# Kernel tuning notes

Hardware: AMD Instinct MI355X
Metric: run time of the kernel (lower is better)

Reference implementation:

```python
import jax, jax.numpy as jnp
import numpy as np

BETA = 0.9
THRESHOLD = 1.0


def setup_inputs() -> dict:
    key = jax.random.key(0)
    k1, k2 = jax.random.split(key)
    T, N_IN, N_OUT = 1024, 4096, 4096
    x = jax.random.normal(k1, (T, N_IN), dtype=jnp.float32)
    # fc1 weight initialized uniform[0,1), shape [out, in] like nn.Linear
    W = jax.random.uniform(k2, (N_OUT, N_IN), dtype=jnp.float32)
    return {"x": x, "W": W}


def reference(x, W):
    # Precompute the batched linear projection over all timesteps: [T, N_OUT]
    cur = jnp.einsum('ti,oi->to', x, W)
    mem0 = jnp.zeros((W.shape[0],), dtype=x.dtype)

    def step(mem, c):
        # snntorch Leaky, reset_mechanism='subtract':
        # reset is computed from the PREVIOUS membrane potential (detached)
        reset = (mem > THRESHOLD).astype(mem.dtype)
        mem_new = BETA * mem + c - reset * THRESHOLD
        spk = (mem_new > THRESHOLD).astype(mem.dtype)
        return mem_new, (spk, mem_new)

    _, (spk_rec, mem_rec) = jax.lax.scan(step, mem0, cur)
    return spk_rec, mem_rec
```

## Files before the change

kernel.cpp:

```cpp
#include <hip/hip_runtime.h>
#include <hip/hip_bf16.h>
#include <stdint.h>


typedef __attribute__((ext_vector_type(8))) short bf16x8;
typedef __attribute__((ext_vector_type(4))) float floatx4;

#define T_STEPS 1024
#define N_IN    4096
#define N_OUT   4096

#define GM 64
#define GN 128
#define BKK 64

#define CHUNK 32
#define NCHUNK (T_STEPS / CHUNK)

#define PH_T 128
#define NB_N 16
#define TP   130

#define TN ((size_t)T_STEPS * N_OUT)

__device__ __forceinline__ unsigned short f2bf_rne(float f) {
    unsigned int u = __builtin_bit_cast(unsigned int, f);
    unsigned int r = 0x7FFFu + ((u >> 16) & 1u);
    return (unsigned short)((u + r) >> 16);
}

__global__ __launch_bounds__(256) void cvt_kernel(const float4* __restrict__ in,
                                                  ushort4* __restrict__ out, int n4) {
    int i = blockIdx.x * blockDim.x + threadIdx.x;
    if (i < n4) {
        float4 v = in[i];
        ushort4 o;
        o.x = f2bf_rne(v.x);
        o.y = f2bf_rne(v.y);
        o.z = f2bf_rne(v.z);
        o.w = f2bf_rne(v.w);
        out[i] = o;
    }
}

__device__ __forceinline__ void gload16(const void* g, void* l) {
    __builtin_amdgcn_global_load_lds((const __attribute__((address_space(1))) void*)g,
                                     (__attribute__((address_space(3))) void*)l,
                                     16, 0, 0);
}

__global__ __launch_bounds__(256) void gemm_bt(const short* __restrict__ A,
                                               const short* __restrict__ B,
                                               float* __restrict__ P,
                                               int kLen) {
    __shared__ short sA[GM * BKK];
    __shared__ short sB[GN * BKK];

    const int tid  = threadIdx.x;
    const int lane = tid & 63;
    const int wv   = tid >> 6;
    const int wn   = wv * 32;

    const int bid    = blockIdx.x;
    const int z      = bid >> 9;
    const int n_tile = bid & 31;
    const int m_tile = (bid >> 5) & 15;
    const long bm = (long)m_tile * GM;
    const long bn = (long)n_tile * GN;
    const int kBeg = z * kLen;
    const int kEnd = kBeg + kLen;
    float* __restrict__ Pz = P + (size_t)z * TN;

    floatx4 acc[4][2] = {};

    const int srow = tid >> 3;
    const int scol = (tid & 7) * 8;
    const short* gA[2];
    const short* gB[4];
    short* lA[2];
    short* lB[4];
#pragma unroll
    for (int p = 0; p < 2; ++p) {
        gA[p] = A + (bm + p * 32 + srow) * (long)N_IN + scol;
        lA[p] = sA + p * 2048 + tid * 8;
    }
#pragma unroll
    for (int p = 0; p < 4; ++p) {
        gB[p] = B + (bn + p * 32 + srow) * (long)N_IN + scol;
        lB[p] = sB + p * 2048 + tid * 8;
    }

    const int fm  = lane & 15;
    const int fko = (lane >> 4) * 8;

    for (int k0 = kBeg; k0 < kEnd; k0 += BKK) {
#pragma unroll
        for (int p = 0; p < 2; ++p) gload16(gA[p] + k0, lA[p]);
#pragma unroll
        for (int p = 0; p < 4; ++p) gload16(gB[p] + k0, lB[p]);
        __syncthreads();

#pragma unroll
        for (int ks = 0; ks < 2; ++ks) {
            bf16x8 af[4], bfr[2];
#pragma unroll
            for (int i = 0; i < 4; ++i)
                af[i] = *(const bf16x8*)(sA + (i * 16 + fm) * 64 + ks * 32 + fko);
#pragma unroll
            for (int j = 0; j < 2; ++j)
                bfr[j] = *(const bf16x8*)(sB + (wn + j * 16 + fm) * 64 + ks * 32 + fko);
#pragma unroll
            for (int i = 0; i < 4; ++i)
#pragma unroll
                for (int j = 0; j < 2; ++j)
                    acc[i][j] = __builtin_amdgcn_mfma_f32_16x16x32_bf16(
                        af[i], bfr[j], acc[i][j], 0, 0, 0);
        }
        __syncthreads();
    }

    const int cn = lane & 15;
    const int cm = (lane >> 4) * 4;
#pragma unroll
    for (int i = 0; i < 4; ++i)
#pragma unroll
        for (int j = 0; j < 2; ++j)
#pragma unroll
            for (int r = 0; r < 4; ++r)
                Pz[(bm + i * 16 + cm + r) * (long)N_OUT + bn + wn + j * 16 + cn] =
                    acc[i][j][r];
}

template <int NPART>
__global__ __launch_bounds__(256) void boundary_kernel(const float* __restrict__ P,
                                                       float* __restrict__ bnd) {
    __shared__ float ring[2][NB_N * TP];

    const int tid  = threadIdx.x;
    const int wv   = tid >> 6;
    const int lane = tid & 63;
    const int n0   = blockIdx.x * NB_N;

    const int pn = lane & 15;
    const int tr = lane >> 4;

    float mem = 0.0f;

    if (wv < 3) {
        float v0[11], v1[11];
        int gidx[11];
#pragma unroll
        for (int i = 0; i < 11; ++i) {
            int g = wv + 3 * i;
            gidx[i] = g;
            if (g < 32) {
                size_t idx = (size_t)(g * 4 + tr) * N_OUT + n0 + pn;
                v0[i] = P[idx];
                if (NPART == 2) v1[i] = P[TN + idx];
            }
        }
#pragma unroll
        for (int i = 0; i < 11; ++i)
            if (gidx[i] < 32)
                ring[0][pn * TP + gidx[i] * 4 + tr] =
                    (NPART == 2) ? (v0[i] + v1[i]) : v0[i];
    }
    __syncthreads();

    for (int ph = 0; ph < T_STEPS / PH_T; ++ph) {
        if (wv < 3) {
            if (ph + 1 < T_STEPS / PH_T) {
                const size_t tb = (size_t)(ph + 1) * PH_T;
                float v0[11], v1[11];
                int gidx[11];
#pragma unroll
                for (int i = 0; i < 11; ++i) {
                    int g = wv + 3 * i;
                    gidx[i] = g;
                    if (g < 32) {
                        size_t idx = (tb + g * 4 + tr) * N_OUT + n0 + pn;
                        v0[i] = P[idx];
                        if (NPART == 2) v1[i] = P[TN + idx];
                    }
                }
#pragma unroll
                for (int i = 0; i < 11; ++i)
                    if (gidx[i] < 32)
                        ring[(ph + 1) & 1][pn * TP + gidx[i] * 4 + tr] =
                            (NPART == 2) ? (v0[i] + v1[i]) : v0[i];
            }
        } else {
            const float* base = &ring[ph & 1][pn * TP];
#pragma unroll
            for (int sub = 0; sub < 4; ++sub) {
                if (lane < 16)
                    bnd[(size_t)(ph * 4 + sub) * N_OUT + n0 + pn] = mem;
                float2 buf[16];
#pragma unroll
                for (int q = 0; q < 16; ++q)
                    buf[q] = *(const float2*)&base[sub * 32 + q * 2];
#pragma unroll
                for (int q = 0; q < 16; ++q) {
                    {
                        float rst = mem > 1.0f ? 1.0f : 0.0f;
                        mem = fmaf(0.9f, mem, buf[q].x) - rst;
                    }
                    {
                        float rst = mem > 1.0f ? 1.0f : 0.0f;
                        mem = fmaf(0.9f, mem, buf[q].y) - rst;
                    }
                }
            }
        }
        __syncthreads();
    }
}

template <int NPART>
__global__ __launch_bounds__(256) void replay_kernel(const float* __restrict__ P,
                                                     const float* __restrict__ bnd,
                                                     float* __restrict__ out) {
    const int lane = threadIdx.x & 63;
    const int w    = threadIdx.x >> 6;
    const int n    = blockIdx.x * 64 + lane;
    const int c    = blockIdx.y * 4 + w;
    float* __restrict__ spk  = out;
    float* __restrict__ memo = out + TN;

    float mem = bnd[(size_t)c * N_OUT + n];
    const float* __restrict__ p0 = P + (size_t)c * CHUNK * N_OUT + n;
    const float* __restrict__ p1 = p0 + TN;

    float v[CHUNK];
#pragma unroll
    for (int j = 0; j < CHUNK; ++j) {
        float a = p0[(size_t)j * N_OUT];
        if (NPART == 2) a += p1[(size_t)j * N_OUT];
        v[j] = a;
    }

#pragma unroll
    for (int j = 0; j < CHUNK; ++j) {
        float rst = mem > 1.0f ? 1.0f : 0.0f;
        mem = fmaf(0.9f, mem, v[j]) - rst;
        size_t idx = (size_t)(c * CHUNK + j) * N_OUT + n;
        spk[idx]  = mem > 1.0f ? 1.0f : 0.0f;
        memo[idx] = mem;
    }
}

extern "C" void kernel_launch(void* const* d_in, const int* in_sizes, int n_in,
                              void* d_out, int out_size, void* d_ws, size_t ws_size,
                              hipStream_t stream) {
    const float* x = (const float*)d_in[0];
    const float* W = (const float*)d_in[1];
    float* out = (float*)d_out;

    char* ws = (char*)d_ws;
    const size_t xbBytes = (size_t)T_STEPS * N_IN * 2;
    const size_t WbBytes = (size_t)N_OUT * N_IN * 2;
    const size_t PBytes  = TN * 4;
    const size_t bndBytes = (size_t)NCHUNK * N_OUT * 4;
    short* xb = (short*)ws;
    short* Wb = (short*)(ws + xbBytes);
    float* P  = (float*)(ws + xbBytes + WbBytes);

    const int S = (ws_size >= xbBytes + WbBytes + 2 * PBytes + bndBytes) ? 2 : 1;
    float* bnd = (float*)(ws + xbBytes + WbBytes + (size_t)S * PBytes);

    {
        int n4 = T_STEPS * N_IN / 4;
        cvt_kernel<<<n4 / 256, 256, 0, stream>>>((const float4*)x, (ushort4*)xb, n4);
    }
    {
        int n4 = N_OUT * N_IN / 4;
        cvt_kernel<<<n4 / 256, 256, 0, stream>>>((const float4*)W, (ushort4*)Wb, n4);
    }

    gemm_bt<<<512 * S, 256, 0, stream>>>(xb, Wb, P, N_IN / S);

    if (S == 2) {
        boundary_kernel<2><<<N_OUT / NB_N, 256, 0, stream>>>(P, bnd);
        replay_kernel<2><<<dim3(N_OUT / 64, NCHUNK / 4), 256, 0, stream>>>(P, bnd, out);
    } else {
        boundary_kernel<1><<<N_OUT / NB_N, 256, 0, stream>>>(P, bnd);
        replay_kernel<1><<<dim3(N_OUT / 64, NCHUNK / 4), 256, 0, stream>>>(P, bnd, out);
    }
}
```

Baseline: 203.2 us.

## Fuse boundary scan and replay into one scan kernel writing outputs directly

The separate boundary and replay kernels are merged into a single scan kernel. Scan lanes store each membrane value into a shared-memory ring, and loader waves write spike and membrane outputs for the previous phase while they prefetch the next phase. This removes the second read of P, the boundary buffer and one launch. Split-K is also raised to 4 partitions when the workspace allows, which gives the GEMM more blocks but means the scan has to read and sum more partial buffers. Output writes are now issued by only 3 waves per block of 16 columns, with stores 16 floats wide, which may give poorly coalesced write bandwidth.

```diff
diff --git a/kernel.cpp b/kernel.cpp
--- a/kernel.cpp
+++ b/kernel.cpp
@@ -14,10 +14,8 @@
 #define GN 128
 #define BKK 64
 
-#define CHUNK 32
-#define NCHUNK (T_STEPS / CHUNK)
-
 #define PH_T 128
+#define NPH  (T_STEPS / PH_T)
 #define NB_N 16
 #define TP   130
 
@@ -132,9 +130,10 @@
 }
 
 template <int NPART>
-__global__ __launch_bounds__(256) void boundary_kernel(const float* __restrict__ P,
-                                                       float* __restrict__ bnd) {
-    __shared__ float ring[2][NB_N * TP];
+__global__ __launch_bounds__(256) void scan_kernel(const float* __restrict__ P,
+                                                   float* __restrict__ out) {
+    __shared__ float ringCur[2][NB_N * TP];
+    __shared__ float ringMem[2][NB_N * TP];
 
     const int tid  = threadIdx.x;
     const int wv   = tid >> 6;
@@ -147,105 +146,116 @@
     float mem = 0.0f;
 
     if (wv < 3) {
-        float v0[11], v1[11];
-        int gidx[11];
+        float v[NPART][11];
+        int gi[11];
 #pragma unroll
         for (int i = 0; i < 11; ++i) {
             int g = wv + 3 * i;
-            gidx[i] = g;
+            gi[i] = g;
             if (g < 32) {
                 size_t idx = (size_t)(g * 4 + tr) * N_OUT + n0 + pn;
-                v0[i] = P[idx];
-                if (NPART == 2) v1[i] = P[TN + idx];
+#pragma unroll
+                for (int zz = 0; zz < NPART; ++zz) v[zz][i] = P[(size_t)zz * TN + idx];
             }
         }
 #pragma unroll
         for (int i = 0; i < 11; ++i)
-            if (gidx[i] < 32)
-                ring[0][pn * TP + gidx[i] * 4 + tr] =
-                    (NPART == 2) ? (v0[i] + v1[i]) : v0[i];
+            if (gi[i] < 32) {
+                float s = v[0][i];
+#pragma unroll
+                for (int zz = 1; zz < NPART; ++zz) s += v[zz][i];
+                ringCur[0][pn * TP + gi[i] * 4 + tr] = s;
+            }
     }
     __syncthreads();
 
-    for (int ph = 0; ph < T_STEPS / PH_T; ++ph) {
+    for (int ph = 0; ph < NPH; ++ph) {
         if (wv < 3) {
-            if (ph + 1 < T_STEPS / PH_T) {
-                const size_t tb = (size_t)(ph + 1) * PH_T;
-                float v0[11], v1[11];
-                int gidx[11];
+            if (ph >= 1) {
+                const float* mr = ringMem[(ph - 1) & 1];
+                const size_t tb = (size_t)(ph - 1) * PH_T;
+                float mv[11];
+                int gi[11];
 #pragma unroll
                 for (int i = 0; i < 11; ++i) {
                     int g = wv + 3 * i;
-                    gidx[i] = g;
+                    gi[i] = g;
+                    if (g < 32) mv[i] = mr[pn * TP + g * 4 + tr];
+                }
+#pragma unroll
+                for (int i = 0; i < 11; ++i)
+                    if (gi[i] < 32) {
+                        size_t idx = (tb + gi[i] * 4 + tr) * N_OUT + n0 + pn;
+                        out[idx]      = mv[i] > 1.0f ? 1.0f : 0.0f;
+                        out[TN + idx] = mv[i];
+                    }
+            }
+            if (ph + 1 < NPH) {
+                const size_t tb = (size_t)(ph + 1) * PH_T;
+                float v[NPART][11];
+                int gi[11];
+#pragma unroll
+                for (int i = 0; i < 11; ++i) {
+                    int g = wv + 3 * i;
+                    gi[i] = g;
                     if (g < 32) {
                         size_t idx = (tb + g * 4 + tr) * N_OUT + n0 + pn;
-                        v0[i] = P[idx];
-                        if (NPART == 2) v1[i] = P[TN + idx];
+#pragma unroll
+                        for (int zz = 0; zz < NPART; ++zz)
+                            v[zz][i] = P[(size_t)zz * TN + idx];
                     }
                 }
 #pragma unroll
                 for (int i = 0; i < 11; ++i)
-                    if (gidx[i] < 32)
-                        ring[(ph + 1) & 1][pn * TP + gidx[i] * 4 + tr] =
-                            (NPART == 2) ? (v0[i] + v1[i]) : v0[i];
-            }
-        } else {
-            const float* base = &ring[ph & 1][pn * TP];
+                    if (gi[i] < 32) {
+                        float s = v[0][i];
+#pragma unroll
+                        for (int zz = 1; zz < NPART; ++zz) s += v[zz][i];
+                        ringCur[(ph + 1) & 1][pn * TP + gi[i] * 4 + tr] = s;
+                    }
+            }
+        } else if (lane < 16) {
+            const float* base = &ringCur[ph & 1][pn * TP];
+            float* mbase = &ringMem[ph & 1][pn * TP];
 #pragma unroll
             for (int sub = 0; sub < 4; ++sub) {
-                if (lane < 16)
-                    bnd[(size_t)(ph * 4 + sub) * N_OUT + n0 + pn] = mem;
                 float2 buf[16];
 #pragma unroll
                 for (int q = 0; q < 16; ++q)
                     buf[q] = *(const float2*)&base[sub * 32 + q * 2];
 #pragma unroll
                 for (int q = 0; q < 16; ++q) {
-                    {
-                        float rst = mem > 1.0f ? 1.0f : 0.0f;
-                        mem = fmaf(0.9f, mem, buf[q].x) - rst;
-                    }
-                    {
-                        float rst = mem > 1.0f ? 1.0f : 0.0f;
-                        mem = fmaf(0.9f, mem, buf[q].y) - rst;
-                    }
+                    float rst = mem > 1.0f ? 1.0f : 0.0f;
+                    mem = fmaf(0.9f, mem, buf[q].x) - rst;
+                    float m0 = mem;
+                    rst = mem > 1.0f ? 1.0f : 0.0f;
+                    mem = fmaf(0.9f, mem, buf[q].y) - rst;
+                    float2 mo; mo.x = m0; mo.y = mem;
+                    *(float2*)&mbase[sub * 32 + q * 2] = mo;
                 }
             }
         }
         __syncthreads();
     }
-}
-
-template <int NPART>
-__global__ __launch_bounds__(256) void replay_kernel(const float* __restrict__ P,
-                                                     const float* __restrict__ bnd,
-                                                     float* __restrict__ out) {
-    const int lane = threadIdx.x & 63;
-    const int w    = threadIdx.x >> 6;
-    const int n    = blockIdx.x * 64 + lane;
-    const int c    = blockIdx.y * 4 + w;
-    float* __restrict__ spk  = out;
-    float* __restrict__ memo = out + TN;
-
-    float mem = bnd[(size_t)c * N_OUT + n];
-    const float* __restrict__ p0 = P + (size_t)c * CHUNK * N_OUT + n;
-    const float* __restrict__ p1 = p0 + TN;
-
-    float v[CHUNK];
-#pragma unroll
-    for (int j = 0; j < CHUNK; ++j) {
-        float a = p0[(size_t)j * N_OUT];
-        if (NPART == 2) a += p1[(size_t)j * N_OUT];
-        v[j] = a;
-    }
-
-#pragma unroll
-    for (int j = 0; j < CHUNK; ++j) {
-        float rst = mem > 1.0f ? 1.0f : 0.0f;
-        mem = fmaf(0.9f, mem, v[j]) - rst;
-        size_t idx = (size_t)(c * CHUNK + j) * N_OUT + n;
-        spk[idx]  = mem > 1.0f ? 1.0f : 0.0f;
-        memo[idx] = mem;
+
+    if (wv < 3) {
+        const float* mr = ringMem[(NPH - 1) & 1];
+        const size_t tb = (size_t)(NPH - 1) * PH_T;
+        float mv[11];
+        int gi[11];
+#pragma unroll
+        for (int i = 0; i < 11; ++i) {
+            int g = wv + 3 * i;
+            gi[i] = g;
+            if (g < 32) mv[i] = mr[pn * TP + g * 4 + tr];
+        }
+#pragma unroll
+        for (int i = 0; i < 11; ++i)
+            if (gi[i] < 32) {
+                size_t idx = (tb + gi[i] * 4 + tr) * N_OUT + n0 + pn;
+                out[idx]      = mv[i] > 1.0f ? 1.0f : 0.0f;
+                out[TN + idx] = mv[i];
+            }
     }
 }
 
@@ -260,13 +270,13 @@
     const size_t xbBytes = (size_t)T_STEPS * N_IN * 2;
     const size_t WbBytes = (size_t)N_OUT * N_IN * 2;
     const size_t PBytes  = TN * 4;
-    const size_t bndBytes = (size_t)NCHUNK * N_OUT * 4;
     short* xb = (short*)ws;
     short* Wb = (short*)(ws + xbBytes);
     float* P  = (float*)(ws + xbBytes + WbBytes);
 
-    const int S = (ws_size >= xbBytes + WbBytes + 2 * PBytes + bndBytes) ? 2 : 1;
-    float* bnd = (float*)(ws + xbBytes + WbBytes + (size_t)S * PBytes);
+    int S = 1;
+    if (ws_size >= xbBytes + WbBytes + 4 * PBytes)      S = 4;
+    else if (ws_size >= xbBytes + WbBytes + 2 * PBytes) S = 2;
 
     {
         int n4 = T_STEPS * N_IN / 4;
@@ -279,11 +289,7 @@
 
     gemm_bt<<<512 * S, 256, 0, stream>>>(xb, Wb, P, N_IN / S);
 
-    if (S == 2) {
-        boundary_kernel<2><<<N_OUT / NB_N, 256, 0, stream>>>(P, bnd);
-        replay_kernel<2><<<dim3(N_OUT / 64, NCHUNK / 4), 256, 0, stream>>>(P, bnd, out);
-    } else {
-        boundary_kernel<1><<<N_OUT / NB_N, 256, 0, stream>>>(P, bnd);
-        replay_kernel<1><<<dim3(N_OUT / 64, NCHUNK / 4), 256, 0, stream>>>(P, bnd, out);
-    }
-}
+    if (S == 4)      scan_kernel<4><<<N_OUT / NB_N, 256, 0, stream>>>(P, out);
+    else if (S == 2) scan_kernel<2><<<N_OUT / NB_N, 256, 0, stream>>>(P, out);
+    else             scan_kernel<1><<<N_OUT / NB_N, 256, 0, stream>>>(P, out);
+}
```

Result: slower. 208.0 us (+2.3%).
